# Kernel tuning notes

Hardware: AMD Instinct MI355X
Metric: run time of the kernel (lower is better)

## Reference

```python
import jax, jax.numpy as jnp
import numpy as np

NUM_LAYERS = 3


def setup_inputs() -> dict:
    key = jax.random.key(0)
    k1, k2, k3 = jax.random.split(key, 3)
    N, D, E = 100000, 64, 1250000
    emb = jax.random.normal(k1, (N, D), dtype=jnp.float32)
    edge_attr = jax.random.uniform(k2, (E,), dtype=jnp.float32)
    edge_index = jax.random.randint(k3, (2, E), 0, N, dtype=jnp.int64)
    return {"emb": emb, "edge_attr": edge_attr, "edge_index": edge_index}


def reference(emb, edge_attr, edge_index):
    # LightGCN.get_embedding with uniform alpha = 1/(num_layers+1)
    N = emb.shape[0]
    src, dst = edge_index[0], edge_index[1]
    # gcn_norm (add_self_loops=False): symmetric normalization of edge weights
    deg = jax.ops.segment_sum(edge_attr, dst, num_segments=N)  # [N]
    dinv = jnp.where(deg > 0, jax.lax.rsqrt(deg), 0.0)
    w = dinv[src] * edge_attr * dinv[dst]  # [E]
    alpha = jnp.float32(1.0 / (NUM_LAYERS + 1))
    x = emb
    out = x * alpha
    for _ in range(NUM_LAYERS):
        # gather source embeddings, scale by normalized weight, scatter-add to dst
        msgs = x[src] * w[:, None]  # [E, D]
        x = jax.ops.segment_sum(msgs, dst, num_segments=N)  # [N, D]
        out = out + x * alpha
    return out
```

## Files before the change

### kernel.cpp

```cpp
#include <hip/hip_runtime.h>
#include <hip/hip_fp16.h>


#define G 256
#define SH 9
#define BNODES 512
#define WINV (1.0f / 32767.0f)

__global__ void __launch_bounds__(256) k_hist(const int* __restrict__ ei,
                                              unsigned int* __restrict__ gcur,
                                              int* __restrict__ chunkbase,
                                              int NB, int E) {
    extern __shared__ unsigned int hist[];
    int g = blockIdx.x, t = threadIdx.x;
    for (int b = t; b < NB; b += 256) hist[b] = 0;
    __syncthreads();
    int chunk = (E + G - 1) / G;
    int lo = g * chunk;
    int hi = min(lo + chunk, E);
    for (int i = lo + t; i < hi; i += 256) {
        int d = ei[E + i];
        atomicAdd(&hist[d >> SH], 1u);
    }
    __syncthreads();
    for (int b = t; b < NB; b += 256) {
        unsigned h = hist[b];
        unsigned base = atomicAdd(&gcur[b], h);
        chunkbase[(size_t)g * NB + b] = (int)base;
    }
}

__global__ void __launch_bounds__(256) k_bscatter(const int* __restrict__ ei,
                                                  const float* __restrict__ ea,
                                                  const unsigned int* __restrict__ gcur,
                                                  const int* __restrict__ chunkbase,
                                                  int2* __restrict__ ebuf, int NB, int E) {
    extern __shared__ unsigned int cur[];
    __shared__ int tot[256];
    int g = blockIdx.x, t = threadIdx.x;
    tot[t] = (t < NB) ? (int)gcur[t] : 0;
    __syncthreads();
    for (int off = 1; off < 256; off <<= 1) {
        int x = (t >= off) ? tot[t - off] : 0;
        __syncthreads();
        tot[t] += x;
        __syncthreads();
    }
    for (int b = t; b < NB; b += 256)
        cur[b] = (unsigned)(tot[b] - (int)gcur[b] + chunkbase[(size_t)g * NB + b]);
    __syncthreads();
    int chunk = (E + G - 1) / G;
    int lo = g * chunk;
    int hi = min(lo + chunk, E);
    for (int i = lo + t; i < hi; i += 256) {
        int srcv = ei[i];
        int d = ei[E + i];
        float w = ea[i];
        unsigned pos = atomicAdd(&cur[d >> SH], 1u);
        int2 m;
        m.x = srcv | ((d & (BNODES - 1)) << 17);
        m.y = __float_as_int(w);
        ebuf[pos] = m;
    }
}

__global__ void __launch_bounds__(512) k_bfinal(const int2* __restrict__ ebuf,
                                                const unsigned int* __restrict__ gcur,
                                                const float2* __restrict__ emb2,
                                                unsigned int* __restrict__ meta,
                                                int* __restrict__ row_start,
                                                float* __restrict__ dinv,
                                                __half2* __restrict__ z0,
                                                int NB, int N, int E) {
    __shared__ int tot[256];
    __shared__ unsigned int hcnt[BNODES];
    __shared__ int sbuf[BNODES];
    __shared__ unsigned int cur[BNODES];
    __shared__ unsigned int hq[BNODES];
    __shared__ float sdv[BNODES];
    int b = blockIdx.x, t = threadIdx.x;

    if (t < 256) tot[t] = (t < NB) ? (int)gcur[t] : 0;
    __syncthreads();
    for (int off = 1; off < 256; off <<= 1) {
        int x = (t < 256 && t >= off) ? tot[t - off] : 0;
        __syncthreads();
        if (t < 256) tot[t] += x;
        __syncthreads();
    }
    int e1 = tot[b];
    int e0 = e1 - (int)gcur[b];

    hcnt[t] = 0;
    hq[t] = 0;
    __syncthreads();
    for (int i = e0 + t; i < e1; i += 512) {
        int2 m = ebuf[i];
        atomicAdd(&hcnt[(m.x >> 17) & (BNODES - 1)], 1u);
    }
    __syncthreads();
    sbuf[t] = (int)hcnt[t];
    __syncthreads();
    for (int off = 1; off < BNODES; off <<= 1) {
        int x = (t >= off) ? sbuf[t - off] : 0;
        __syncthreads();
        sbuf[t] += x;
        __syncthreads();
    }
    int excl = sbuf[t] - (int)hcnt[t];
    cur[t] = (unsigned)excl;
    int node = (b << SH) + t;
    if (node < N) row_start[node] = e0 + excl;
    if (b == 0 && t == 0) row_start[N] = E;
    __syncthreads();
    for (int i = e0 + t; i < e1; i += 512) {
        int2 m = ebuf[i];
        int dl = (m.x >> 17) & (BNODES - 1);
        unsigned p = atomicAdd(&cur[dl], 1u);
        float w = __int_as_float(m.y);
        unsigned q = (unsigned)__float2int_rn(w * 32767.0f);
        q = min(q, 32767u);
        atomicAdd(&hq[dl], q);
        meta[e0 + (int)p] = (unsigned)(m.x & ((1 << 17) - 1)) | (q << 17);
    }
    __syncthreads();
    float s = (float)hq[t] * WINV;
    float dv = (s > 0.0f) ? rsqrtf(s) : 0.0f;
    sdv[t] = dv;
    if (node < N) dinv[node] = dv;
    __syncthreads();
    int base = b << SH;
    for (int idx = t; idx < BNODES * 32; idx += 512) {
        int nd = idx >> 5;
        int gnode = base + nd;
        if (gnode < N) {
            float sc = sdv[nd];
            float2 v = emb2[(size_t)gnode * 32 + (idx & 31)];
            z0[(size_t)gnode * 32 + (idx & 31)] = __floats2half2_rn(v.x * sc, v.y * sc);
        }
    }
}

union F2H {
    float2 f;
    __half2 h[2];
};

template <int MODE>
__global__ void __launch_bounds__(256) k_prop(const float2* __restrict__ zin,
                                              const unsigned int* __restrict__ meta,
                                              const int* __restrict__ row_start,
                                              const float* __restrict__ dinv,
                                              float2* __restrict__ zout,
                                              const float4* __restrict__ emb,
                                              const float2* __restrict__ z1,
                                              const float2* __restrict__ z2,
                                              float4* __restrict__ out, int N) {
    int g = (blockIdx.x * 256 + threadIdx.x) >> 4;
    if (g >= N) return;
    int l = threadIdx.x & 15;
    int b = row_start[g];
    int e = row_start[g + 1];

    float4 acc = make_float4(0.f, 0.f, 0.f, 0.f);
    int i = b;
    for (; i + 8 <= e; i += 8) {
        unsigned mm[8];
        F2H uu[8];
        #pragma unroll
        for (int k = 0; k < 8; ++k) mm[k] = meta[i + k];
        #pragma unroll
        for (int k = 0; k < 8; ++k) uu[k].f = zin[(size_t)(mm[k] & 0x1FFFFu) * 16 + l];
        #pragma unroll
        for (int k = 0; k < 8; ++k) {
            float w = (float)(mm[k] >> 17) * WINV;
            float2 a = __half22float2(uu[k].h[0]), bb = __half22float2(uu[k].h[1]);
            acc.x = fmaf(a.x, w, acc.x);
            acc.y = fmaf(a.y, w, acc.y);
            acc.z = fmaf(bb.x, w, acc.z);
            acc.w = fmaf(bb.y, w, acc.w);
        }
    }
    for (; i + 4 <= e; i += 4) {
        unsigned mm[4];
        F2H uu[4];
        #pragma unroll
        for (int k = 0; k < 4; ++k) mm[k] = meta[i + k];
        #pragma unroll
        for (int k = 0; k < 4; ++k) uu[k].f = zin[(size_t)(mm[k] & 0x1FFFFu) * 16 + l];
        #pragma unroll
        for (int k = 0; k < 4; ++k) {
            float w = (float)(mm[k] >> 17) * WINV;
            float2 a = __half22float2(uu[k].h[0]), bb = __half22float2(uu[k].h[1]);
            acc.x = fmaf(a.x, w, acc.x);
            acc.y = fmaf(a.y, w, acc.y);
            acc.z = fmaf(bb.x, w, acc.z);
            acc.w = fmaf(bb.y, w, acc.w);
        }
    }
    for (; i < e; ++i) {
        unsigned m = meta[i];
        F2H u;
        u.f = zin[(size_t)(m & 0x1FFFFu) * 16 + l];
        float w = (float)(m >> 17) * WINV;
        float2 a = __half22float2(u.h[0]), bb = __half22float2(u.h[1]);
        acc.x = fmaf(a.x, w, acc.x);
        acc.y = fmaf(a.y, w, acc.y);
        acc.z = fmaf(bb.x, w, acc.z);
        acc.w = fmaf(bb.y, w, acc.w);
    }

    float sd = dinv[g];
    int o = g * 16 + l;
    if (MODE == 0) {
        float s2 = sd * sd;
        F2H u;
        u.h[0] = __floats2half2_rn(s2 * acc.x, s2 * acc.y);
        u.h[1] = __floats2half2_rn(s2 * acc.z, s2 * acc.w);
        zout[o] = u.f;
    } else {
        float rd = (sd > 0.0f) ? (1.0f / sd) : 0.0f;
        F2H u1, u2;
        u1.f = z1[o];
        u2.f = z2[o];
        float2 a1 = __half22float2(u1.h[0]), b1 = __half22float2(u1.h[1]);
        float2 a2 = __half22float2(u2.h[0]), b2 = __half22float2(u2.h[1]);
        float4 ev = emb[o];
        float4 r;
        r.x = 0.25f * (ev.x + rd * (a1.x + a2.x) + sd * acc.x);
        r.y = 0.25f * (ev.y + rd * (a1.y + a2.y) + sd * acc.y);
        r.z = 0.25f * (ev.z + rd * (b1.x + b2.x) + sd * acc.z);
        r.w = 0.25f * (ev.w + rd * (b1.y + b2.y) + sd * acc.w);
        out[o] = r;
    }
}

static inline size_t align_up(size_t x, size_t a) { return (x + a - 1) & ~(a - 1); }

extern "C" void kernel_launch(void* const* d_in, const int* in_sizes, int n_in,
                              void* d_out, int out_size, void* d_ws, size_t ws_size,
                              hipStream_t stream) {
    const float* emb = (const float*)d_in[0];
    const float* ea  = (const float*)d_in[1];
    const int*   ei  = (const int*)d_in[2];
    float* out = (float*)d_out;

    const int D = 64;
    const int N = in_sizes[0] / D;
    const int E = in_sizes[1];

    const int NB = (N + BNODES - 1) / BNODES;

    char* ws = (char*)d_ws;
    size_t off = 0;
    unsigned int* gcur = (unsigned int*)(ws + off);
                                            off = align_up(off + (size_t)NB * 4, 256);
    int* chunkbase = (int*)(ws + off);      off = align_up(off + (size_t)G * NB * 4, 256);
    int* row_start = (int*)(ws + off);      off = align_up(off + (size_t)(N + 1) * 4, 256);
    float* dinv = (float*)(ws + off);       off = align_up(off + (size_t)N * 4, 256);
    int2* ebuf = (int2*)(ws + off);         off = align_up(off + (size_t)E * 8, 256);
    unsigned int* meta = (unsigned int*)(ws + off); off = align_up(off + (size_t)E * 4, 256);
    __half2* z0 = (__half2*)(ws + off);     off = align_up(off + (size_t)N * D * 2, 256);
    __half2* z1 = (__half2*)(ws + off);     off = align_up(off + (size_t)N * D * 2, 256);
    __half2* z2 = (__half2*)(ws + off);     off = align_up(off + (size_t)N * D * 2, 256);
    (void)ws_size;

    hipMemsetAsync(gcur, 0, (size_t)NB * 4, stream);
    k_hist<<<G, 256, NB * 4, stream>>>(ei, gcur, chunkbase, NB, E);
    k_bscatter<<<G, 256, NB * 4, stream>>>(ei, ea, gcur, chunkbase, ebuf, NB, E);
    k_bfinal<<<NB, 512, 0, stream>>>(ebuf, gcur, (const float2*)emb, meta, row_start,
                                     dinv, z0, NB, N, E);

    int lb = (N * 16 + 255) / 256;
    k_prop<0><<<lb, 256, 0, stream>>>((const float2*)z0, meta, row_start, dinv,
                                      (float2*)z1, nullptr, nullptr, nullptr, nullptr, N);
    k_prop<0><<<lb, 256, 0, stream>>>((const float2*)z1, meta, row_start, dinv,
                                      (float2*)z2, nullptr, nullptr, nullptr, nullptr, N);
    k_prop<1><<<lb, 256, 0, stream>>>((const float2*)z2, meta, row_start, dinv,
                                      nullptr, (const float4*)emb, (const float2*)z1,
                                      (const float2*)z2, (float4*)out, N);
}
```

Measured before the change: 142.8 us.

## Halve CSR bucket size and stage bucket edges in LDS during finalize

Shrinks each destination bucket from 512 to 256 nodes, which doubles the bucket count to about 391 and the number of finalize blocks. The bucket scatter kernel moves to 512 threads so its scan can cover the larger bucket count. In the finalize kernel, a bucket's edges are loaded once into an LDS staging buffer (up to 6144 entries, about 48 KB) and reused for the histogram and placement passes instead of reading global memory twice. Weight sums for the degree are now computed in the histogram pass, which lets dinv be ready before placement. The larger LDS footprint may lower occupancy, and buckets that overflow the staging buffer take a global fallback path.

After: 140.3 us, median of 2. No clear change (-1.8%).

```diff
diff --git a/kernel.cpp b/kernel.cpp
--- a/kernel.cpp
+++ b/kernel.cpp
@@ -3,8 +3,9 @@
 
 
 #define G 256
-#define SH 9
-#define BNODES 512
+#define SH 8
+#define BNODES 256
+#define CAP 6144
 #define WINV (1.0f / 32767.0f)
 
 __global__ void __launch_bounds__(256) k_hist(const int* __restrict__ ei,
@@ -30,29 +31,29 @@
     }
 }
 
-__global__ void __launch_bounds__(256) k_bscatter(const int* __restrict__ ei,
+__global__ void __launch_bounds__(512) k_bscatter(const int* __restrict__ ei,
                                                   const float* __restrict__ ea,
                                                   const unsigned int* __restrict__ gcur,
                                                   const int* __restrict__ chunkbase,
                                                   int2* __restrict__ ebuf, int NB, int E) {
+    __shared__ int tot[512];
     extern __shared__ unsigned int cur[];
-    __shared__ int tot[256];
     int g = blockIdx.x, t = threadIdx.x;
     tot[t] = (t < NB) ? (int)gcur[t] : 0;
     __syncthreads();
-    for (int off = 1; off < 256; off <<= 1) {
+    for (int off = 1; off < 512; off <<= 1) {
         int x = (t >= off) ? tot[t - off] : 0;
         __syncthreads();
         tot[t] += x;
         __syncthreads();
     }
-    for (int b = t; b < NB; b += 256)
+    for (int b = t; b < NB; b += 512)
         cur[b] = (unsigned)(tot[b] - (int)gcur[b] + chunkbase[(size_t)g * NB + b]);
     __syncthreads();
     int chunk = (E + G - 1) / G;
     int lo = g * chunk;
     int hi = min(lo + chunk, E);
-    for (int i = lo + t; i < hi; i += 256) {
+    for (int i = lo + t; i < hi; i += 512) {
         int srcv = ei[i];
         int d = ei[E + i];
         float w = ea[i];
@@ -72,62 +73,119 @@
                                                 float* __restrict__ dinv,
                                                 __half2* __restrict__ z0,
                                                 int NB, int N, int E) {
-    __shared__ int tot[256];
+    __shared__ int tot[512];
+    __shared__ int2 estage[CAP];
     __shared__ unsigned int hcnt[BNODES];
     __shared__ int sbuf[BNODES];
-    __shared__ unsigned int cur[BNODES];
+    __shared__ unsigned int cur2[BNODES];
     __shared__ unsigned int hq[BNODES];
     __shared__ float sdv[BNODES];
     int b = blockIdx.x, t = threadIdx.x;
 
-    if (t < 256) tot[t] = (t < NB) ? (int)gcur[t] : 0;
-    __syncthreads();
-    for (int off = 1; off < 256; off <<= 1) {
-        int x = (t < 256 && t >= off) ? tot[t - off] : 0;
-        __syncthreads();
-        if (t < 256) tot[t] += x;
+    tot[t] = (t < NB) ? (int)gcur[t] : 0;
+    __syncthreads();
+    for (int off = 1; off < 512; off <<= 1) {
+        int x = (t >= off) ? tot[t - off] : 0;
+        __syncthreads();
+        tot[t] += x;
         __syncthreads();
     }
     int e1 = tot[b];
     int e0 = e1 - (int)gcur[b];
-
-    hcnt[t] = 0;
-    hq[t] = 0;
-    __syncthreads();
-    for (int i = e0 + t; i < e1; i += 512) {
-        int2 m = ebuf[i];
-        atomicAdd(&hcnt[(m.x >> 17) & (BNODES - 1)], 1u);
-    }
-    __syncthreads();
-    sbuf[t] = (int)hcnt[t];
-    __syncthreads();
-    for (int off = 1; off < BNODES; off <<= 1) {
-        int x = (t >= off) ? sbuf[t - off] : 0;
-        __syncthreads();
-        sbuf[t] += x;
-        __syncthreads();
-    }
-    int excl = sbuf[t] - (int)hcnt[t];
-    cur[t] = (unsigned)excl;
-    int node = (b << SH) + t;
-    if (node < N) row_start[node] = e0 + excl;
+    int cnt = e1 - e0;
+
+    if (t < BNODES) {
+        hcnt[t] = 0;
+        hq[t] = 0;
+    }
+    __syncthreads();
+
+    if (cnt <= CAP) {
+        for (int i = t; i < cnt; i += 512) estage[i] = ebuf[e0 + i];
+        __syncthreads();
+        for (int i = t; i < cnt; i += 512) {
+            int2 m = estage[i];
+            int dl = (m.x >> 17) & (BNODES - 1);
+            float w = __int_as_float(m.y);
+            unsigned q = (unsigned)__float2int_rn(w * 32767.0f);
+            q = min(q, 32767u);
+            atomicAdd(&hcnt[dl], 1u);
+            atomicAdd(&hq[dl], q);
+        }
+        __syncthreads();
+        if (t < BNODES) sbuf[t] = (int)hcnt[t];
+        __syncthreads();
+        for (int off = 1; off < BNODES; off <<= 1) {
+            int x = (t < BNODES && t >= off) ? sbuf[t - off] : 0;
+            __syncthreads();
+            if (t < BNODES) sbuf[t] += x;
+            __syncthreads();
+        }
+        int node = (b << SH) + t;
+        if (t < BNODES) {
+            int excl = sbuf[t] - (int)hcnt[t];
+            cur2[t] = (unsigned)excl;
+            float s = (float)hq[t] * WINV;
+            float dv = (s > 0.0f) ? rsqrtf(s) : 0.0f;
+            sdv[t] = dv;
+            if (node < N) {
+                row_start[node] = e0 + excl;
+                dinv[node] = dv;
+            }
+        }
+        __syncthreads();
+        for (int i = t; i < cnt; i += 512) {
+            int2 m = estage[i];
+            int dl = (m.x >> 17) & (BNODES - 1);
+            unsigned p = atomicAdd(&cur2[dl], 1u);
+            float w = __int_as_float(m.y);
+            unsigned q = (unsigned)__float2int_rn(w * 32767.0f);
+            q = min(q, 32767u);
+            meta[e0 + (int)p] = (unsigned)(m.x & ((1 << 17) - 1)) | (q << 17);
+        }
+    } else {
+        for (int i = e0 + t; i < e1; i += 512) {
+            int2 m = ebuf[i];
+            int dl = (m.x >> 17) & (BNODES - 1);
+            float w = __int_as_float(m.y);
+            unsigned q = (unsigned)__float2int_rn(w * 32767.0f);
+            q = min(q, 32767u);
+            atomicAdd(&hcnt[dl], 1u);
+            atomicAdd(&hq[dl], q);
+        }
+        __syncthreads();
+        if (t < BNODES) sbuf[t] = (int)hcnt[t];
+        __syncthreads();
+        for (int off = 1; off < BNODES; off <<= 1) {
+            int x = (t < BNODES && t >= off) ? sbuf[t - off] : 0;
+            __syncthreads();
+            if (t < BNODES) sbuf[t] += x;
+            __syncthreads();
+        }
+        int node = (b << SH) + t;
+        if (t < BNODES) {
+            int excl = sbuf[t] - (int)hcnt[t];
+            cur2[t] = (unsigned)excl;
+            float s = (float)hq[t] * WINV;
+            float dv = (s > 0.0f) ? rsqrtf(s) : 0.0f;
+            sdv[t] = dv;
+            if (node < N) {
+                row_start[node] = e0 + excl;
+                dinv[node] = dv;
+            }
+        }
+        __syncthreads();
+        for (int i = e0 + t; i < e1; i += 512) {
+            int2 m = ebuf[i];
+            int dl = (m.x >> 17) & (BNODES - 1);
+            unsigned p = atomicAdd(&cur2[dl], 1u);
+            float w = __int_as_float(m.y);
+            unsigned q = (unsigned)__float2int_rn(w * 32767.0f);
+            q = min(q, 32767u);
+            meta[e0 + (int)p] = (unsigned)(m.x & ((1 << 17) - 1)) | (q << 17);
+        }
+    }
     if (b == 0 && t == 0) row_start[N] = E;
-    __syncthreads();
-    for (int i = e0 + t; i < e1; i += 512) {
-        int2 m = ebuf[i];
-        int dl = (m.x >> 17) & (BNODES - 1);
-        unsigned p = atomicAdd(&cur[dl], 1u);
-        float w = __int_as_float(m.y);
-        unsigned q = (unsigned)__float2int_rn(w * 32767.0f);
-        q = min(q, 32767u);
-        atomicAdd(&hq[dl], q);
-        meta[e0 + (int)p] = (unsigned)(m.x & ((1 << 17) - 1)) | (q << 17);
-    }
-    __syncthreads();
-    float s = (float)hq[t] * WINV;
-    float dv = (s > 0.0f) ? rsqrtf(s) : 0.0f;
-    sdv[t] = dv;
-    if (node < N) dinv[node] = dv;
     __syncthreads();
     int base = b << SH;
     for (int idx = t; idx < BNODES * 32; idx += 512) {
@@ -267,7 +325,7 @@
 
     hipMemsetAsync(gcur, 0, (size_t)NB * 4, stream);
     k_hist<<<G, 256, NB * 4, stream>>>(ei, gcur, chunkbase, NB, E);
-    k_bscatter<<<G, 256, NB * 4, stream>>>(ei, ea, gcur, chunkbase, ebuf, NB, E);
+    k_bscatter<<<G, 512, NB * 4, stream>>>(ei, ea, gcur, chunkbase, ebuf, NB, E);
     k_bfinal<<<NB, 512, 0, stream>>>(ebuf, gcur, (const float2*)emb, meta, row_start,
                                      dinv, z0, NB, N, E);
 
```
